# Optimization experiments

Measured on AMD Instinct MI355X. Metric: run time of the kernel, lower is better.

Reference implementation:

```python
import jax, jax.numpy as jnp
import numpy as np

NUM_CLASSES = 80
SOFT_CENTER_RADIUS = 3.0
TOPK = 13
IOU_WEIGHT = 3.0
EPS = 1e-7
IOU_EPS = 1e-6
INF = 1e8


def _pairwise_iou(boxes, gts):
    # boxes: [B,N,4] xyxy, gts: [B,M,4] xyxy -> [B,N,M]
    lt = jnp.maximum(boxes[:, :, None, :2], gts[:, None, :, :2])
    rb = jnp.minimum(boxes[:, :, None, 2:], gts[:, None, :, 2:])
    wh = jnp.clip(rb - lt, 0.0)
    inter = wh[..., 0] * wh[..., 1]
    a1 = (boxes[..., 2] - boxes[..., 0]) * (boxes[..., 3] - boxes[..., 1])
    a2 = (gts[..., 2] - gts[..., 0]) * (gts[..., 3] - gts[..., 1])
    union = jnp.maximum(a1[:, :, None] + a2[:, None, :] - inter, IOU_EPS)
    return inter / union


def setup_inputs() -> dict:
    key = jax.random.key(0)
    ks = jax.random.split(key, 6)
    B, M, C, size = 32, 60, NUM_CLASSES, 640
    # grid priors for strides 8/16/32 -> N = 6400+1600+400 = 8400
    pr = []
    for s in (8, 16, 32):
        n = size // s
        ys, xs = jnp.meshgrid(jnp.arange(n) * s + s / 2.0,
                              jnp.arange(n) * s + s / 2.0, indexing='ij')
        pr.append(jnp.stack([xs.ravel(), ys.ravel(),
                             jnp.full((n * n,), float(s)),
                             jnp.full((n * n,), float(s))], -1))
    priors = jnp.concatenate(pr, 0).astype(jnp.float32)  # [8400,4]
    N = priors.shape[0]

    def make_boxes(k, b, m, wmin, wmax):
        c = jax.random.uniform(k, (b, m, 2), minval=0.0, maxval=float(size))
        wh = jax.random.uniform(jax.random.fold_in(k, 1), (b, m, 2),
                                minval=wmin, maxval=wmax)
        return jnp.concatenate([c - wh / 2, c + wh / 2], -1).astype(jnp.float32)

    pred_bboxes = make_boxes(ks[0], B, N, 5.0, 200.0)
    gt_bboxes = make_boxes(ks[1], B, M, 20.0, 200.0)
    pred_scores = (jax.random.normal(ks[2], (B, N, C)) * 2.0).astype(jnp.float32)
    gt_labels = jax.random.randint(ks[3], (B, M, 1), 0, C)
    nvalid = jax.random.randint(ks[4], (B,), 1, M + 1)
    pad_bbox_flag = (jnp.arange(M)[None, :] < nvalid[:, None]).astype(jnp.float32)[..., None]
    return dict(pred_bboxes=pred_bboxes, pred_scores=pred_scores, priors=priors,
                gt_labels=gt_labels, gt_bboxes=gt_bboxes, pad_bbox_flag=pad_bbox_flag)


def reference(pred_bboxes, pred_scores, priors, gt_labels, gt_bboxes, pad_bbox_flag):
    B, N, _ = pred_bboxes.shape
    M = gt_bboxes.shape[1]

    # --- inside-box mask (box_dim == 4) ---
    pc = priors[:, :2]  # [N,2]
    lt = pc[:, None, None] - gt_bboxes[..., :2]        # [N,B,M,2]
    rb = gt_bboxes[..., 2:] - pc[:, None, None]        # [N,B,M,2]
    is_in = jnp.min(jnp.concatenate([lt, rb], -1), -1) > 0  # [N,B,M]
    is_in = is_in * pad_bbox_flag[..., 0][None]        # mask padded gts
    is_in = jnp.transpose(is_in, (1, 0, 2))            # [B,N,M]
    valid_mask = is_in.sum(-1) > 0                     # [B,N]

    # --- soft center prior ---
    gt_center = (gt_bboxes[..., :2] + gt_bboxes[..., 2:]) / 2.0  # [B,M,2]
    strides = priors[:, 2]
    dist = jnp.sqrt(((pc[None, :, None, :] - gt_center[:, None, :, :]) ** 2).sum(-1)) \
        / strides[None, :, None]                       # [B,N,M]
    dist = dist * valid_mask[..., None]
    soft_center_prior = 10.0 ** (dist - SOFT_CENTER_RADIUS)

    # --- iou cost ---
    pairwise_ious = _pairwise_iou(pred_bboxes, gt_bboxes)  # [B,N,M]
    iou_cost = -jnp.log(pairwise_ious + EPS) * IOU_WEIGHT

    # --- cls cost: gather per-gt class logits ---
    labels = gt_labels[..., 0].astype(jnp.int32)        # [B,M]
    pw_logits = jnp.take_along_axis(
        pred_scores, jnp.broadcast_to(labels[:, None, :], (B, N, M)), axis=2)
    scale = pairwise_ious - jax.nn.sigmoid(pw_logits)
    bce = jnp.maximum(pw_logits, 0.0) - pw_logits * pairwise_ious \
        + jnp.log1p(jnp.exp(-jnp.abs(pw_logits)))       # stable BCE-with-logits
    cls_cost = bce * jnp.abs(scale) ** 2

    cost = cls_cost + iou_cost + soft_center_prior
    cost = jnp.where(valid_mask[..., None], cost, INF)

    # --- dynamic k matching ---
    k = min(TOPK, N)
    topk_ious = jax.lax.top_k(jnp.swapaxes(pairwise_ious, 1, 2), k)[0]  # [B,M,k]
    dynamic_ks = jnp.maximum(topk_ious.sum(-1).astype(jnp.int32), 1)    # [B,M]
    # rank of each prior within each gt column (ascending cost)
    rank = jnp.argsort(jnp.argsort(cost, axis=1), axis=1)               # [B,N,M]
    gt_valid = pad_bbox_flag[..., 0] > 0                                # [B,M]
    matching = (rank < dynamic_ks[:, None, :]) & gt_valid[:, None, :]   # [B,N,M] bool
    # resolve priors matched to >1 gt: keep min-cost gt
    multi = matching.sum(-1) > 1                                        # [B,N]
    amin = jnp.argmin(cost, axis=-1)                                    # [B,N]
    onehot = jnp.arange(M)[None, None, :] == amin[..., None]
    matching = jnp.where(multi[..., None], onehot, matching)
    fg_mask = matching.sum(-1) > 0                                      # [B,N]
    matched_gt_inds = jnp.argmax(matching, -1)                          # [B,N]
    matched_pred_ious = (matching * pairwise_ious).sum(-1)              # [B,N]

    # --- assemble outputs ---
    labels_g = jnp.take_along_axis(gt_labels[..., 0], matched_gt_inds, axis=1)
    assigned_labels = jnp.where(fg_mask, labels_g, NUM_CLASSES).astype(jnp.int32)
    assigned_labels_weights = jnp.ones((B, N), dtype=gt_bboxes.dtype)
    boxes_g = jnp.take_along_axis(gt_bboxes, matched_gt_inds[..., None], axis=1)
    assigned_bboxes = jnp.where(fg_mask[..., None], boxes_g, 0.0)
    assign_metrics = jnp.where(fg_mask, matched_pred_ious, 0.0)
    return (assigned_labels, assigned_labels_weights, assigned_bboxes, assign_metrics)
```

## Files before the change

### kernel.cpp

```cpp
#include <hip/hip_runtime.h>
#include <hip/hip_bf16.h>
#include <math.h>

#define B 32
#define N 8400
#define M 60
#define C 80
#define INF_COST 1e8f
#define NPART 4
#define PLEN 2100
#define PJ 9

typedef unsigned long long u64;

__device__ __forceinline__ float iou_fn(
    float px1, float py1, float px2, float py2,
    float gx1, float gy1, float gx2, float gy2)
{
#pragma clang fp contract(off)
    float ltx = fmaxf(px1, gx1), lty = fmaxf(py1, gy1);
    float rbx = fminf(px2, gx2), rby = fminf(py2, gy2);
    float wx = fmaxf(rbx - ltx, 0.0f), wy = fmaxf(rby - lty, 0.0f);
    float inter = wx * wy;
    float a1 = (px2 - px1) * (py2 - py1);
    float a2 = (gx2 - gx1) * (gy2 - gy1);
    float uni = fmaxf(a1 + a2 - inter, 1e-6f);
    return inter / uni;
}

__device__ __forceinline__ float cost_fast(
    float iou, float logit,
    float pcx, float pcy, float rstride,
    float gcx, float gcy)
{
#pragma clang fp contract(off)
    const float LOG2_10 = 3.3219280948873623f;
    const float LOG2_E  = 1.4426950408889634f;
    const float LN_2    = 0.6931471805599453f;
    float dx = pcx - gcx, dy = pcy - gcy;
    float dist = __builtin_amdgcn_sqrtf(dx * dx + dy * dy) * rstride;
    float soft = __builtin_amdgcn_exp2f((dist - 3.0f) * LOG2_10);
    float iouc = __builtin_amdgcn_logf(iou + 1e-7f) * (-3.0f * LN_2);
    float e    = __builtin_amdgcn_exp2f(-logit * LOG2_E);
    float sig  = __builtin_amdgcn_rcpf(1.0f + e);
    float t    = __builtin_amdgcn_exp2f(-fabsf(logit) * LOG2_E);
    float sp   = __builtin_amdgcn_logf(1.0f + t) * LN_2;
    float bce  = fmaxf(logit, 0.0f) - logit * iou + sp;
    float scale = iou - sig;
    float cls  = bce * scale * scale;
    return (cls + iouc) + soft;
}

__device__ __forceinline__ u64 wave_sort_asc(u64 key, int lane)
{
#pragma unroll
    for (int k = 2; k <= 64; k <<= 1) {
#pragma unroll
        for (int j = k >> 1; j > 0; j >>= 1) {
            u64 o = __shfl_xor((unsigned long long)key, j);
            bool keepmin = ((lane & k) == 0) == ((lane & j) == 0);
            bool take = (o < key) == keepmin;
            if (take) key = o;
        }
    }
    return key;
}

__global__ __launch_bounds__(256) void k_valid(
    const float* __restrict__ priors,
    const float* __restrict__ gt_bboxes,
    const float* __restrict__ pad,
    unsigned char* __restrict__ valid)
{
    int idx = blockIdx.x * 256 + threadIdx.x;
    if (idx >= B * N) return;
    int b = idx / N, n = idx % N;
    float px = priors[n * 4 + 0];
    float py = priors[n * 4 + 1];
    const float* g = gt_bboxes + (size_t)b * M * 4;
    const float* pf = pad + (size_t)b * M;
    unsigned char v = 0;
    for (int m = 0; m < M; m++) {
        float x1 = g[m * 4 + 0], y1 = g[m * 4 + 1];
        float x2 = g[m * 4 + 2], y2 = g[m * 4 + 3];
        float mn = fminf(fminf(px - x1, py - y1), fminf(x2 - px, y2 - py));
        if (mn > 0.0f && pf[m] > 0.0f) { v = 1; break; }
    }
    valid[idx] = v;
}

__global__ __launch_bounds__(256) void k_part(
    const float* __restrict__ pred_bboxes,
    const float* __restrict__ pred_scores,
    const float* __restrict__ priors,
    const int*   __restrict__ gt_labels,
    const float* __restrict__ gt_bboxes,
    const float* __restrict__ pad,
    const unsigned char* __restrict__ valid,
    float* __restrict__ PI, float* __restrict__ PC, int* __restrict__ PN)
{
    __shared__ u64      s_ckey[4][13];
    __shared__ u64      s_ikey[4][13];
    __shared__ u64      s_thr[2];
    __shared__ float    s_cv[160]; __shared__ int s_cn[160];
    __shared__ float    s_iv[160]; __shared__ int s_in[160];
    __shared__ unsigned s_cnt[2];
    __shared__ float    s_slotc[13]; __shared__ int s_slotn[13];
    __shared__ float    s_sloti[13];

    const int i = blockIdx.x;
    const int bm = i >> 2, part = i & 3;
    if (pad[bm] == 0.0f) return;

    const int b = bm / M;
    const int tid = threadIdx.x;
    const int lane = tid & 63;
    const int w = tid >> 6;
    const int base = part * PLEN;

    if (tid == 0) { s_cnt[0] = 0; s_cnt[1] = 0; }

    const float4 g = ((const float4*)gt_bboxes)[bm];
    const float gx1 = g.x, gy1 = g.y, gx2 = g.z, gy2 = g.w;
    const float gcx = (gx1 + gx2) * 0.5f, gcy = (gy1 + gy2) * 0.5f;
    const int label = gt_labels[bm];
    const float4* pb4 = ((const float4*)pred_bboxes) + (size_t)b * N;
    const float* srow = pred_scores + (size_t)b * N * C;
    const unsigned char* vrow = valid + (size_t)b * N;
    const float4* pr4 = (const float4*)priors;

    float myi[PJ], myc[PJ];
    u64 minc = ~0ull, maxi = ~0ull;

#pragma unroll
    for (int j = 0; j < PJ; ++j) {
        int off = tid + (j << 8);
        float v = 0.0f, c = 0.0f;
        if (off < PLEN) {
            int n = base + off;
            float4 p = pb4[n];
            v = iou_fn(p.x, p.y, p.z, p.w, gx1, gy1, gx2, gy2);
            if (vrow[n]) {
                float4 pr = pr4[n];
                c = cost_fast(v, srow[(size_t)n * C + label], pr.x, pr.y,
                              __builtin_amdgcn_rcpf(pr.z), gcx, gcy);
            } else c = INF_COST;
            u64 ck = ((u64)__float_as_uint(c) << 32) | (unsigned)n;
            if (ck < minc) minc = ck;
            u64 ik = ((u64)(0xFFFFFFFFu - __float_as_uint(v)) << 32) | (unsigned)n;
            if (ik < maxi) maxi = ik;
        }
        myi[j] = v; myc[j] = c;
    }

    {
        u64 sc = wave_sort_asc(minc, lane);
        if (lane < 13) s_ckey[w][lane] = sc;
        u64 si = wave_sort_asc(maxi, lane);
        if (lane < 13) s_ikey[w][lane] = si;
    }
    __syncthreads();

    if (tid < 2) {
        const u64 (*L)[13] = (tid == 0) ? s_ckey : s_ikey;
        int q0 = 0, q1 = 0, q2 = 0, q3 = 0;
        u64 t = 0;
        for (int r = 0; r < 13; ++r) {
            u64 v0 = L[0][q0], v1 = L[1][q1], v2 = L[2][q2], v3 = L[3][q3];
            u64 bv = v0; int bw = 0;
            if (v1 < bv) { bv = v1; bw = 1; }
            if (v2 < bv) { bv = v2; bw = 2; }
            if (v3 < bv) { bv = v3; bw = 3; }
            t = bv;
            if (bw == 0) q0++; else if (bw == 1) q1++; else if (bw == 2) q2++; else q3++;
        }
        s_thr[tid] = t;
    }
    __syncthreads();
    const u64 tc = s_thr[0];
    const u64 ti = s_thr[1];

#pragma unroll
    for (int j = 0; j < PJ; ++j) {
        int off = tid + (j << 8);
        if (off < PLEN) {
            int n = base + off;
            u64 ck = ((u64)__float_as_uint(myc[j]) << 32) | (unsigned)n;
            if (ck <= tc) {
                unsigned p = atomicAdd(&s_cnt[0], 1u);
                if (p < 160u) { s_cv[p] = myc[j]; s_cn[p] = n; }
            }
            u64 ik = ((u64)(0xFFFFFFFFu - __float_as_uint(myi[j])) << 32) | (unsigned)n;
            if (ik <= ti) {
                unsigned p = atomicAdd(&s_cnt[1], 1u);
                if (p < 160u) { s_iv[p] = myi[j]; s_in[p] = n; }
            }
        }
    }
    __syncthreads();

    {
        const unsigned nc = s_cnt[0], ng = s_cnt[1];
        if (tid < 128) {
            unsigned ii = tid;
            if (ii < nc) {
                float c = s_cv[ii]; int nn = s_cn[ii];
                unsigned r = 0;
                for (unsigned t = 0; t < nc; ++t) {
                    float u = s_cv[t];
                    r += (u < c || (u == c && s_cn[t] < nn)) ? 1u : 0u;
                }
                if (r < 13u) { s_slotc[r] = c; s_slotn[r] = nn; }
            }
        } else {
            unsigned ii = tid - 128;
            if (ii < ng) {
                float v = s_iv[ii]; int nn = s_in[ii];
                unsigned r = 0;
                for (unsigned t = 0; t < ng; ++t) {
                    float u = s_iv[t];
                    r += (u > v || (u == v && s_in[t] < nn)) ? 1u : 0u;
                }
                if (r < 13u) s_sloti[r] = v;
            }
        }
    }
    __syncthreads();

    if (tid < 13) {
        int o = (bm * NPART + part) * 13 + tid;
        PC[o] = s_slotc[tid];
        PN[o] = s_slotn[tid];
        PI[o] = s_sloti[tid];
    }
}

__global__ __launch_bounds__(256) void k_merge(
    const float* __restrict__ pad,
    const float* __restrict__ PI,
    const float* __restrict__ PC,
    const int*   __restrict__ PN,
    float* __restrict__ cK, int* __restrict__ nK)
{
    int bm = blockIdx.x * 256 + threadIdx.x;
    if (bm >= B * M) return;
    if (pad[bm] == 0.0f) return;

    const float* pi = PI + (size_t)bm * 52;
    const float* pc = PC + (size_t)bm * 52;
    const int*   pn = PN + (size_t)bm * 52;

    int q0 = 0, q1 = 0, q2 = 0, q3 = 0;
    float ss = 0.0f;
    for (int r = 0; r < 13; ++r) {
        float v0 = (q0 < 13) ? pi[q0]      : -1.0f;
        float v1 = (q1 < 13) ? pi[13 + q1] : -1.0f;
        float v2 = (q2 < 13) ? pi[26 + q2] : -1.0f;
        float v3 = (q3 < 13) ? pi[39 + q3] : -1.0f;
        float bv = v0; int bw = 0;
        if (v1 > bv) { bv = v1; bw = 1; }
        if (v2 > bv) { bv = v2; bw = 2; }
        if (v3 > bv) { bv = v3; bw = 3; }
        ss += bv;
        if (bw == 0) q0++; else if (bw == 1) q1++; else if (bw == 2) q2++; else q3++;
    }
    int K = (int)ss;
    if (K < 1) K = 1;

    q0 = q1 = q2 = q3 = 0;
    float ck = 0.0f; int nk = 0;
    for (int r = 0; r < K; ++r) {
        float c0 = (q0 < 13) ? pc[q0]      : INFINITY; int n0 = (q0 < 13) ? pn[q0]      : 0x7fffffff;
        float c1 = (q1 < 13) ? pc[13 + q1] : INFINITY; int n1 = (q1 < 13) ? pn[13 + q1] : 0x7fffffff;
        float c2 = (q2 < 13) ? pc[26 + q2] : INFINITY; int n2 = (q2 < 13) ? pn[26 + q2] : 0x7fffffff;
        float c3 = (q3 < 13) ? pc[39 + q3] : INFINITY; int n3 = (q3 < 13) ? pn[39 + q3] : 0x7fffffff;
        float bv = c0; int bn = n0, bw = 0;
        if (c1 < bv || (c1 == bv && n1 < bn)) { bv = c1; bn = n1; bw = 1; }
        if (c2 < bv || (c2 == bv && n2 < bn)) { bv = c2; bn = n2; bw = 2; }
        if (c3 < bv || (c3 == bv && n3 < bn)) { bv = c3; bn = n3; bw = 3; }
        ck = bv; nk = bn;
        if (bw == 0) q0++; else if (bw == 1) q1++; else if (bw == 2) q2++; else q3++;
    }
    cK[bm] = ck; nK[bm] = nk;
}

__global__ __launch_bounds__(256) void k_assign(
    const float* __restrict__ pred_bboxes,
    const float* __restrict__ pred_scores,
    const float* __restrict__ priors,
    const int*   __restrict__ gt_labels,
    const float* __restrict__ gt_bboxes,
    const float* __restrict__ pad,
    const unsigned char* __restrict__ valid,
    const float* __restrict__ cK,
    const int*   __restrict__ nK,
    float* __restrict__ out)
{
    __shared__ float s_box[M][4];
    __shared__ float s_gc[M][2];
    __shared__ float s_ck[M];
    __shared__ int   s_lab[M];
    __shared__ int   s_nk[M];
    __shared__ unsigned char s_gtv[M];

    const int cidx = blockIdx.x;
    const int b = cidx / 33;
    const int chunk = cidx % 33;
    const int n = chunk * 256 + threadIdx.x;

    if (threadIdx.x < M) {
        int m = threadIdx.x, gi = b * M + m;
        float4 g = ((const float4*)gt_bboxes)[gi];
        s_box[m][0] = g.x; s_box[m][1] = g.y; s_box[m][2] = g.z; s_box[m][3] = g.w;
        s_gc[m][0] = (g.x + g.z) * 0.5f;
        s_gc[m][1] = (g.y + g.w) * 0.5f;
        s_ck[m] = cK[gi];
        s_lab[m] = gt_labels[gi];
        s_nk[m] = nK[gi];
        s_gtv[m] = (pad[gi] > 0.0f) ? 1 : 0;
    }
    __syncthreads();
    if (n >= N) return;

    const size_t idx = (size_t)b * N + n;
    const float4 p = ((const float4*)pred_bboxes)[idx];
    const int vn = valid[idx];

    float* o_lab = out;
    float* o_w   = out + (size_t)B * N;
    float* o_box = out + (size_t)2 * B * N;
    float* o_met = out + (size_t)6 * B * N;

    int count = 0, firstm = -1;
    int mstar; float mi;

    if (!vn) {
#pragma unroll
        for (int m = 0; m < M; m++) {
            float ckm = s_ck[m]; int nkm = s_nk[m];
            bool matched = s_gtv[m] &&
                           (INF_COST < ckm || (INF_COST == ckm && n <= nkm));
            if (matched) { count++; if (firstm < 0) firstm = m; }
        }
        mstar = (count > 1) ? 0 : firstm;
        mi = 0.0f;
        if (mstar >= 0)
            mi = iou_fn(p.x, p.y, p.z, p.w,
                        s_box[mstar][0], s_box[mstar][1], s_box[mstar][2], s_box[mstar][3]);
    } else {
        const float4 pr = ((const float4*)priors)[n];
        const float rst = __builtin_amdgcn_rcpf(pr.z);
        const float* scores = pred_scores + idx * C;

        float minc = INFINITY; int amin = 0;
        float firstiou = 0.0f, aminiou = 0.0f;

        for (int mc = 0; mc < 4; ++mc) {
            float lg[15];
#pragma unroll
            for (int t = 0; t < 15; ++t) lg[t] = scores[s_lab[mc * 15 + t]];
#pragma unroll
            for (int t = 0; t < 15; ++t) {
                int m = mc * 15 + t;
                float iou = iou_fn(p.x, p.y, p.z, p.w,
                                   s_box[m][0], s_box[m][1], s_box[m][2], s_box[m][3]);
                float c = cost_fast(iou, lg[t], pr.x, pr.y, rst, s_gc[m][0], s_gc[m][1]);
                if (c < minc) { minc = c; amin = m; aminiou = iou; }
                float ckm = s_ck[m]; int nkm = s_nk[m];
                bool matched = s_gtv[m] && (c < ckm || (c == ckm && n <= nkm));
                if (matched) { count++; if (firstm < 0) { firstm = m; firstiou = iou; } }
            }
        }
        if (count > 1)       { mstar = amin;   mi = aminiou; }
        else if (count == 1) { mstar = firstm; mi = firstiou; }
        else                 { mstar = -1;     mi = 0.0f; }
    }

    o_w[idx] = 1.0f;
    if (mstar >= 0) {
        o_lab[idx] = (float)s_lab[mstar];
        o_box[idx * 4 + 0] = s_box[mstar][0];
        o_box[idx * 4 + 1] = s_box[mstar][1];
        o_box[idx * 4 + 2] = s_box[mstar][2];
        o_box[idx * 4 + 3] = s_box[mstar][3];
        o_met[idx] = mi;
    } else {
        o_lab[idx] = (float)C;
        o_box[idx * 4 + 0] = 0.0f;
        o_box[idx * 4 + 1] = 0.0f;
        o_box[idx * 4 + 2] = 0.0f;
        o_box[idx * 4 + 3] = 0.0f;
        o_met[idx] = 0.0f;
    }
}

extern "C" void kernel_launch(void* const* d_in, const int* in_sizes, int n_in,
                              void* d_out, int out_size, void* d_ws, size_t ws_size,
                              hipStream_t stream) {
    const float* pred_bboxes = (const float*)d_in[0];
    const float* pred_scores = (const float*)d_in[1];
    const float* priors      = (const float*)d_in[2];
    const int*   gt_labels   = (const int*)d_in[3];
    const float* gt_bboxes   = (const float*)d_in[4];
    const float* pad         = (const float*)d_in[5];
    float* out = (float*)d_out;

    unsigned char* ws = (unsigned char*)d_ws;
    size_t off = 0;
    unsigned char* valid = ws;                  off += (size_t)B * N;
    float* cKp = (float*)(ws + off);            off += (size_t)B * M * 4;
    int*   nKp = (int*)(ws + off);              off += (size_t)B * M * 4;
    float* PI  = (float*)(ws + off);            off += (size_t)B * M * NPART * 13 * 4;
    float* PC  = (float*)(ws + off);            off += (size_t)B * M * NPART * 13 * 4;
    int*   PN  = (int*)(ws + off);              off += (size_t)B * M * NPART * 13 * 4;

    k_valid<<<(B * N + 255) / 256, 256, 0, stream>>>(priors, gt_bboxes, pad, valid);
    k_part <<<B * M * NPART, 256, 0, stream>>>(pred_bboxes, pred_scores, priors, gt_labels,
                                               gt_bboxes, pad, valid, PI, PC, PN);
    k_merge<<<(B * M + 255) / 256, 256, 0, stream>>>(pad, PI, PC, PN, cKp, nKp);
    k_assign<<<33 * B, 256, 0, stream>>>(pred_bboxes, pred_scores, priors, gt_labels,
                                         gt_bboxes, pad, valid, cKp, nKp, out);
}
```

Before: 137.9 us.

## Prefilter priors by center-distance bound before full cost loop; use float min tracking

In the assign kernel, each valid prior first checks whether any valid gt is close enough that its cost could fall at or below that gt's top-k threshold. The check uses a distance bound derived from the threshold through the log-based center prior. Only priors that pass load scores and run the full 60-gt IoU/cost loop; the rest are written as background. The top-k kernel also tracks min/max as float+index pairs instead of 64-bit packed keys to reduce integer work. The bound relies on the cost's other terms being non-negative and adds a serial scan over gts per prior, which could mis-skip if that assumption fails.

```diff
diff --git a/kernel.cpp b/kernel.cpp
--- a/kernel.cpp
+++ b/kernel.cpp
@@ -130,7 +130,8 @@
     const float4* pr4 = (const float4*)priors;
 
     float myi[PJ], myc[PJ];
-    u64 minc = ~0ull, maxi = ~0ull;
+    float mcv = INFINITY; int mcn = 0x7fffffff;
+    float mxv = -1.0f;    int mxn = 0x7fffffff;
 
 #pragma unroll
     for (int j = 0; j < PJ; ++j) {
@@ -145,13 +146,14 @@
                 c = cost_fast(v, srow[(size_t)n * C + label], pr.x, pr.y,
                               __builtin_amdgcn_rcpf(pr.z), gcx, gcy);
             } else c = INF_COST;
-            u64 ck = ((u64)__float_as_uint(c) << 32) | (unsigned)n;
-            if (ck < minc) minc = ck;
-            u64 ik = ((u64)(0xFFFFFFFFu - __float_as_uint(v)) << 32) | (unsigned)n;
-            if (ik < maxi) maxi = ik;
+            if (c < mcv) { mcv = c; mcn = n; }
+            if (v > mxv) { mxv = v; mxn = n; }
         }
         myi[j] = v; myc[j] = c;
     }
+
+    u64 minc = ((u64)__float_as_uint(mcv) << 32) | (unsigned)mcn;
+    u64 maxi = ((u64)(0xFFFFFFFFu - __float_as_uint(mxv)) << 32) | (unsigned)mxn;
 
     {
         u64 sc = wave_sort_asc(minc, lane);
@@ -179,19 +181,21 @@
     __syncthreads();
     const u64 tc = s_thr[0];
     const u64 ti = s_thr[1];
+    const float tcv = __uint_as_float((unsigned)(tc >> 32));
+    const int   tcn = (int)(unsigned)(tc & 0xFFFFFFFFu);
+    const float tiv = __uint_as_float(0xFFFFFFFFu - (unsigned)(ti >> 32));
+    const int   tin = (int)(unsigned)(ti & 0xFFFFFFFFu);
 
 #pragma unroll
     for (int j = 0; j < PJ; ++j) {
         int off = tid + (j << 8);
         if (off < PLEN) {
             int n = base + off;
-            u64 ck = ((u64)__float_as_uint(myc[j]) << 32) | (unsigned)n;
-            if (ck <= tc) {
+            if (myc[j] < tcv || (myc[j] == tcv && n <= tcn)) {
                 unsigned p = atomicAdd(&s_cnt[0], 1u);
                 if (p < 160u) { s_cv[p] = myc[j]; s_cn[p] = n; }
             }
-            u64 ik = ((u64)(0xFFFFFFFFu - __float_as_uint(myi[j])) << 32) | (unsigned)n;
-            if (ik <= ti) {
+            if (myi[j] > tiv || (myi[j] == tiv && n <= tin)) {
                 unsigned p = atomicAdd(&s_cnt[1], 1u);
                 if (p < 160u) { s_iv[p] = myi[j]; s_in[p] = n; }
             }
@@ -302,6 +306,7 @@
     __shared__ int   s_lab[M];
     __shared__ int   s_nk[M];
     __shared__ unsigned char s_gtv[M];
+    __shared__ float s_d2[M];
 
     const int cidx = blockIdx.x;
     const int b = cidx / 33;
@@ -317,7 +322,15 @@
         s_ck[m] = cK[gi];
         s_lab[m] = gt_labels[gi];
         s_nk[m] = nK[gi];
-        s_gtv[m] = (pad[gi] > 0.0f) ? 1 : 0;
+        bool gv = (pad[gi] > 0.0f);
+        s_gtv[m] = gv ? 1 : 0;
+        float d2 = -1.0f;
+        if (gv) {
+            float ds = 3.0f + __builtin_amdgcn_logf(cK[gi] + 0.02f) * 0.30102999566398f + 0.01f;
+            ds = fmaxf(ds, 0.0f);
+            d2 = ds * ds;
+        }
+        s_d2[m] = d2;
     }
     __syncthreads();
     if (n >= N) return;
@@ -332,7 +345,7 @@
     float* o_met = out + (size_t)6 * B * N;
 
     int count = 0, firstm = -1;
-    int mstar; float mi;
+    int mstar = -1; float mi = 0.0f;
 
     if (!vn) {
 #pragma unroll
@@ -343,37 +356,46 @@
             if (matched) { count++; if (firstm < 0) firstm = m; }
         }
         mstar = (count > 1) ? 0 : firstm;
-        mi = 0.0f;
         if (mstar >= 0)
             mi = iou_fn(p.x, p.y, p.z, p.w,
                         s_box[mstar][0], s_box[mstar][1], s_box[mstar][2], s_box[mstar][3]);
     } else {
         const float4 pr = ((const float4*)priors)[n];
         const float rst = __builtin_amdgcn_rcpf(pr.z);
-        const float* scores = pred_scores + idx * C;
-
-        float minc = INFINITY; int amin = 0;
-        float firstiou = 0.0f, aminiou = 0.0f;
-
-        for (int mc = 0; mc < 4; ++mc) {
-            float lg[15];
-#pragma unroll
-            for (int t = 0; t < 15; ++t) lg[t] = scores[s_lab[mc * 15 + t]];
-#pragma unroll
-            for (int t = 0; t < 15; ++t) {
-                int m = mc * 15 + t;
-                float iou = iou_fn(p.x, p.y, p.z, p.w,
-                                   s_box[m][0], s_box[m][1], s_box[m][2], s_box[m][3]);
-                float c = cost_fast(iou, lg[t], pr.x, pr.y, rst, s_gc[m][0], s_gc[m][1]);
-                if (c < minc) { minc = c; amin = m; aminiou = iou; }
-                float ckm = s_ck[m]; int nkm = s_nk[m];
-                bool matched = s_gtv[m] && (c < ckm || (c == ckm && n <= nkm));
-                if (matched) { count++; if (firstm < 0) { firstm = m; firstiou = iou; } }
+        const float rs2 = rst * rst;
+
+        bool pot = false;
+        for (int m = 0; m < M; m++) {
+            float dx = pr.x - s_gc[m][0];
+            float dy = pr.y - s_gc[m][1];
+            float q = dx * dx + dy * dy;
+            if (q * rs2 <= s_d2[m]) { pot = true; break; }
+        }
+
+        if (pot) {
+            const float* scores = pred_scores + idx * C;
+            float minc = INFINITY; int amin = 0;
+            float firstiou = 0.0f, aminiou = 0.0f;
+
+            for (int mc = 0; mc < 4; ++mc) {
+                float lg[15];
+#pragma unroll
+                for (int t = 0; t < 15; ++t) lg[t] = scores[s_lab[mc * 15 + t]];
+#pragma unroll
+                for (int t = 0; t < 15; ++t) {
+                    int m = mc * 15 + t;
+                    float iou = iou_fn(p.x, p.y, p.z, p.w,
+                                       s_box[m][0], s_box[m][1], s_box[m][2], s_box[m][3]);
+                    float c = cost_fast(iou, lg[t], pr.x, pr.y, rst, s_gc[m][0], s_gc[m][1]);
+                    if (c < minc) { minc = c; amin = m; aminiou = iou; }
+                    float ckm = s_ck[m]; int nkm = s_nk[m];
+                    bool matched = s_gtv[m] && (c < ckm || (c == ckm && n <= nkm));
+                    if (matched) { count++; if (firstm < 0) { firstm = m; firstiou = iou; } }
+                }
             }
-        }
-        if (count > 1)       { mstar = amin;   mi = aminiou; }
-        else if (count == 1) { mstar = firstm; mi = firstiou; }
-        else                 { mstar = -1;     mi = 0.0f; }
+            if (count > 1)       { mstar = amin;   mi = aminiou; }
+            else if (count == 1) { mstar = firstm; mi = firstiou; }
+        }
     }
 
     o_w[idx] = 1.0f;
```

Result: slower. 142.3 us (+3.1%).
